# Optimization experiments

Hardware: AMD Instinct MI355X
Metric: run time of the kernel (lower is better)

Reference implementation:

```python
import jax, jax.numpy as jnp
import numpy as np

ALPHA_LO = float(np.exp(-1.0 / 5.0))   # 0.8187
ALPHA_HI = float(np.exp(-1.0 / 25.0))  # 0.9608
BN_EPS = 1e-5

B, T, D_IN, H = 32, 2000, 512, 512


def setup_inputs() -> dict:
    key = jax.random.key(0)
    ks = jax.random.split(key, 5)
    x = jax.random.normal(ks[0], (B, T, D_IN), dtype=jnp.float32)
    W = jax.random.normal(ks[1], (H, D_IN), dtype=jnp.float32) / np.sqrt(D_IN)
    b = jax.random.normal(ks[2], (H,), dtype=jnp.float32) * 0.01
    alpha = jax.random.uniform(ks[3], (H,), dtype=jnp.float32,
                               minval=ALPHA_LO, maxval=ALPHA_HI)
    gamma = jnp.ones((H,), dtype=jnp.float32)
    beta = jnp.zeros((H,), dtype=jnp.float32)
    ut0 = jax.random.uniform(ks[4], (B, H), dtype=jnp.float32)
    return {"x": x, "W": W, "b": b, "alpha": alpha,
            "gamma": gamma, "beta": beta, "ut0": ut0}


def reference(x, W, b, alpha, gamma, beta, ut0):
    # Linear: [B,T,Din] @ [Din,H] + b
    Wx = jnp.einsum("btd,hd->bth", x, W) + b
    # BatchNorm1d (training forward): stats over flattened (B*T) dim
    flat = Wx.reshape(-1, Wx.shape[-1])
    mean = flat.mean(axis=0)
    var = flat.var(axis=0)  # biased, as torch BN uses for normalization
    Wx = ((flat - mean) * jax.lax.rsqrt(var + BN_EPS) * gamma + beta).reshape(Wx.shape)
    # Readout cell: leaky integration + softmax accumulation over time
    a = jnp.clip(alpha, ALPHA_LO, ALPHA_HI)

    def step(carry, wxt):
        ut, acc = carry
        ut = a * ut + (1.0 - a) * wxt          # [B,H]
        acc = acc + jax.nn.softmax(ut, axis=1)
        return (ut, acc), None

    wx_t = jnp.transpose(Wx, (1, 0, 2))  # [T,B,H]
    (_, out), _ = jax.lax.scan(step, (ut0, jnp.zeros_like(ut0)), wx_t)
    return out[:, None, :]  # [B,1,H]
```

## Files before the change

### kernel.cpp

```cpp
#include <hip/hip_runtime.h>
#include <hip/hip_bf16.h>
#include <stdint.h>


namespace {
constexpr int kB = 32;
constexpr int kT = 2000;
constexpr int kD = 512;
constexpr int kH = 512;
constexpr int kM = kB * kT;
constexpr int kBM = 64;
constexpr int kNB = kM / kBM;
constexpr int kL = 16;
constexpr int kC = kT / kL;
constexpr int kG = 5;
constexpr int kNG = kC / kG;
constexpr float kALo = 0.81873075307798182f;
constexpr float kAHi = 0.96078943915232320f;

typedef __bf16 bf16x4 __attribute__((ext_vector_type(4)));
typedef __bf16 bf16x8 __attribute__((ext_vector_type(8)));
typedef float floatx16 __attribute__((ext_vector_type(16)));

__device__ __forceinline__ float bf2f(unsigned short u) {
  return __builtin_bit_cast(float, (unsigned)u << 16);
}
__device__ __forceinline__ float clipa(float a) {
  return fminf(fmaxf(a, kALo), kAHi);
}
__device__ __forceinline__ float pow16(float a) {
  const float a2 = a * a, a4 = a2 * a2, a8 = a4 * a4;
  return a8 * a8;
}

__global__ __launch_bounds__(256) void wcvt_k(const float* __restrict__ W,
                                              __bf16* __restrict__ Wbf) {
  const int t = blockIdx.x * 256 + threadIdx.x;
  const float4 a0 = ((const float4*)W)[t * 2];
  const float4 a1 = ((const float4*)W)[t * 2 + 1];
  bf16x8 v;
  v[0] = (__bf16)a0.x; v[1] = (__bf16)a0.y; v[2] = (__bf16)a0.z; v[3] = (__bf16)a0.w;
  v[4] = (__bf16)a1.x; v[5] = (__bf16)a1.y; v[6] = (__bf16)a1.z; v[7] = (__bf16)a1.w;
  const int h = t >> 6, k8 = t & 63;
  *(bf16x8*)(Wbf + ((size_t)k8 * 512 + h) * 8) = v;
}

__global__ __launch_bounds__(512, 4) void gemm_k(const float* __restrict__ X,
                                                 const __bf16* __restrict__ Wbf,
                                                 const float* __restrict__ alpha,
                                                 unsigned short* __restrict__ Wxb,
                                                 float* __restrict__ vbuf,
                                                 float* __restrict__ partial) {
  __shared__ alignas(16) __bf16 As2[2][4][65][8];
  __shared__ float sred[2][kH];
  const int tid = threadIdx.x;
  const size_t row0 = (size_t)blockIdx.x * kBM;
  const int w = tid >> 6, L = tid & 63;
  const int ct0 = w * 2;
  const int lhalf = L >> 5, l32 = L & 31;
  const int arow = tid >> 3, acol = (tid & 7) * 4;
  const int akq = acol >> 3, aoff = acol & 7;

  floatx16 acc[2][2] = {};
  const float* xptr = X + (row0 + arow) * kD + acol;
  const __bf16* bptr = Wbf + ((size_t)(ct0 * 32) + l32) * 8;

  float4 a0 = *(const float4*)xptr;
  {
    bf16x4 av;
    av[0] = (__bf16)a0.x; av[1] = (__bf16)a0.y;
    av[2] = (__bf16)a0.z; av[3] = (__bf16)a0.w;
    *(bf16x4*)&As2[0][akq][arow][aoff] = av;
  }
  a0 = *(const float4*)(xptr + 32);
  asm volatile("s_waitcnt lgkmcnt(0)" ::: "memory");
  __builtin_amdgcn_s_barrier();

#pragma unroll 1
  for (int s = 0; s < 16; ++s) {
    const int buf = s & 1;
    if (s < 15) {
      bf16x4 av;
      av[0] = (__bf16)a0.x; av[1] = (__bf16)a0.y;
      av[2] = (__bf16)a0.z; av[3] = (__bf16)a0.w;
      *(bf16x4*)&As2[buf ^ 1][akq][arow][aoff] = av;
      if (s < 14)
        a0 = *(const float4*)(xptr + (s + 2) * 32);
    }
#pragma unroll
    for (int kh = 0; kh < 2; ++kh) {
      const int kq = kh * 2 + lhalf;
      const __bf16* bq = bptr + (size_t)(s * 4 + kq) * 4096;
      const bf16x8 b0 = *(const bf16x8*)bq;
      const bf16x8 b1 = *(const bf16x8*)(bq + 256);
      const bf16x8 af0 = *(const bf16x8*)&As2[buf][kq][l32][0];
      const bf16x8 af1 = *(const bf16x8*)&As2[buf][kq][32 + l32][0];
      acc[0][0] = __builtin_amdgcn_mfma_f32_32x32x16_bf16(af0, b0, acc[0][0], 0, 0, 0);
      acc[0][1] = __builtin_amdgcn_mfma_f32_32x32x16_bf16(af0, b1, acc[0][1], 0, 0, 0);
      acc[1][0] = __builtin_amdgcn_mfma_f32_32x32x16_bf16(af1, b0, acc[1][0], 0, 0, 0);
      acc[1][1] = __builtin_amdgcn_mfma_f32_32x32x16_bf16(af1, b1, acc[1][1], 0, 0, 0);
    }
    if (s < 15) {
      asm volatile("s_waitcnt lgkmcnt(0)" ::: "memory");
      __builtin_amdgcn_s_barrier();
    }
  }

  __syncthreads();
  sred[0][tid] = 0.f;
  sred[1][tid] = 0.f;
  __syncthreads();
#pragma unroll
  for (int c = 0; c < 2; ++c) {
    float s = 0.f, q = 0.f;
#pragma unroll
    for (int rt = 0; rt < 2; ++rt) {
#pragma unroll
      for (int r = 0; r < 16; ++r) {
        const float v = acc[rt][c][r];
        s += v;
        q += v * v;
      }
    }
    s += __shfl_xor(s, 32);
    q += __shfl_xor(q, 32);
    if (lhalf == 0) {
      atomicAdd(&sred[0][(ct0 + c) * 32 + l32], s);
      atomicAdd(&sred[1][(ct0 + c) * 32 + l32], q);
    }
  }

#pragma unroll
  for (int c = 0; c < 2; ++c) {
    const int col = (ct0 + c) * 32 + l32;
    const float a = clipa(alpha[col]);
    const float oma = 1.0f - a;
    const float a2 = a * a, a4 = a2 * a2, a8 = a4 * a4;
    float wgt[8];
    wgt[0] = a8 * a2 * a; wgt[1] = a8 * a2; wgt[2] = a8 * a; wgt[3] = a8;
    wgt[4] = a2 * a;      wgt[5] = a2;      wgt[6] = a;      wgt[7] = 1.0f;
    const float mult = (lhalf == 0) ? a4 * oma : oma;
#pragma unroll
    for (int j = 0; j < 8; ++j) wgt[j] *= mult;
#pragma unroll
    for (int rt = 0; rt < 2; ++rt) {
#pragma unroll
      for (int c32 = 0; c32 < 2; ++c32) {
        float S = 0.f;
#pragma unroll
        for (int j = 0; j < 8; ++j) S += wgt[j] * acc[rt][c][c32 * 8 + j];
        S += __shfl_xor(S, 32);
        if (lhalf == 0) {
          const int g = (int)blockIdx.x * 4 + rt * 2 + c32;
          vbuf[(size_t)g * kH + col] = S;
        }
      }
    }
  }

#pragma unroll
  for (int rt = 0; rt < 2; ++rt) {
#pragma unroll
    for (int c = 0; c < 2; ++c) {
      const int col = (ct0 + c) * 32 + l32;
#pragma unroll
      for (int r = 0; r < 16; ++r) {
        const int row = rt * 32 + 4 * lhalf + (r & 3) + 8 * (r >> 2);
        const unsigned short u = __builtin_bit_cast(unsigned short, (__bf16)acc[rt][c][r]);
        const unsigned un = __shfl_down((unsigned)u, 1);
        if ((l32 & 1) == 0)
          *(unsigned*)(Wxb + (row0 + row) * (size_t)kH + col) = (unsigned)u | (un << 16);
      }
    }
  }
  __syncthreads();
  partial[(size_t)blockIdx.x * 1024 + tid] = sred[0][tid];
  partial[(size_t)blockIdx.x * 1024 + 512 + tid] = sred[1][tid];
}

__global__ __launch_bounds__(512) void red1_k(const float* __restrict__ partial,
                                              float* __restrict__ sums) {
  const int tid = threadIdx.x;
  const int r0 = blockIdx.x * 25;
  float s0 = 0.f, s1 = 0.f;
#pragma unroll 5
  for (int r = 0; r < 25; ++r) {
    s0 += partial[(size_t)(r0 + r) * 1024 + tid];
    s1 += partial[(size_t)(r0 + r) * 1024 + 512 + tid];
  }
  atomicAdd(&sums[tid], s0);
  atomicAdd(&sums[kH + tid], s1);
}

__global__ __launch_bounds__(512) void fin_scan_k(const float* __restrict__ sums,
                                                  const float* __restrict__ alpha,
                                                  const float* __restrict__ gamma,
                                                  const float* __restrict__ beta,
                                                  const float* __restrict__ ut0,
                                                  float* __restrict__ prm,
                                                  const float* __restrict__ vbuf,
                                                  float* __restrict__ ustart) {
  const int h = threadIdx.x;
  const int b = blockIdx.x;
  const float inv_n = 1.0f / (float)kM;
  const float mean = sums[h] * inv_n;
  const float var = sums[kH + h] * inv_n - mean * mean;
  const float sc = gamma[h] * rsqrtf(var + 1e-5f);
  const float sh = beta[h] - mean * sc;
  const float a = clipa(alpha[h]);
  if (b == 0) {
    prm[h] = sc;
    prm[kH + h] = sh;
    prm[2 * kH + h] = a;
    prm[3 * kH + h] = 1.0f - a;
  }
  const float a16 = pow16(a);
  const float shc = sh * (1.0f - a16);
  float u = ut0[(size_t)b * kH + h];
  float vc[kG];
#pragma unroll 1
  for (int cb = 0; cb < kC; cb += kG) {
#pragma unroll
    for (int j = 0; j < kG; ++j)
      vc[j] = vbuf[((size_t)b * kC + cb + j) * kH + h];
    ustart[((size_t)b * kNG + cb / kG) * kH + h] = u;
#pragma unroll
    for (int j = 0; j < kG; ++j) u = a16 * u + sc * vc[j] + shc;
  }
}

__global__ __launch_bounds__(512) void soft_k(const unsigned short* __restrict__ Wxb,
                                              const float* __restrict__ prm,
                                              const float* __restrict__ ustart,
                                              float* __restrict__ out) {
  __shared__ float part[kL][9];
  __shared__ float zinv[kL];
  const int bc = blockIdx.x;
  const int b = bc / kNG, grp = bc % kNG;
  const int h = threadIdx.x;
  const int wv = h >> 6, lane = h & 63;
  const float sc = prm[h], sh = prm[kH + h];
  const float a = prm[2 * kH + h], oma = prm[3 * kH + h];
  float u = ustart[(size_t)bc * kH + h];
  const unsigned short* base =
      Wxb + ((size_t)b * kT + (size_t)grp * kG * kL) * kH + h;
  float acc = 0.f;
#pragma unroll 1
  for (int cc = 0; cc < kG; ++cc) {
    float e[kL];
#pragma unroll
    for (int i = 0; i < kL; ++i) {
      const float wvx = bf2f(base[(size_t)(cc * kL + i) * kH]) * sc + sh;
      u = a * u + oma * wvx;
      e[i] = __expf(u);
    }
#pragma unroll
    for (int i = 0; i < kL; ++i) {
      float s = e[i];
#pragma unroll
      for (int off = 32; off > 0; off >>= 1) s += __shfl_xor(s, off);
      if (lane == 0) part[i][wv] = s;
    }
    __syncthreads();
    if (h < kL) {
      float s = 0.f;
#pragma unroll
      for (int j = 0; j < 8; ++j) s += part[h][j];
      zinv[h] = 1.0f / s;
    }
    __syncthreads();
#pragma unroll
    for (int i = 0; i < kL; ++i) acc += e[i] * zinv[i];
    __syncthreads();
  }
  atomicAdd(&out[(size_t)b * kH + h], acc);
}

}

extern "C" void kernel_launch(void* const* d_in, const int* in_sizes, int n_in,
                              void* d_out, int out_size, void* d_ws, size_t ws_size,
                              hipStream_t stream) {
  const float* x = (const float*)d_in[0];
  const float* Wm = (const float*)d_in[1];
  const float* alpha = (const float*)d_in[3];
  const float* gamma = (const float*)d_in[4];
  const float* beta = (const float*)d_in[5];
  const float* ut0 = (const float*)d_in[6];
  float* out = (float*)d_out;

  float* wsp = (float*)d_ws;
  float* vbuf = wsp;
  float* ustart = vbuf + (size_t)kB * kC * kH;
  float* partial = ustart + (size_t)kB * kNG * kH;
  float* sums = partial + (size_t)1000 * 1024;
  float* prm = sums + 2 * kH;
  __bf16* Wbf = (__bf16*)(prm + 4 * kH);
  unsigned short* Wxb = (unsigned short*)(Wbf + (size_t)kH * kD);

  hipMemsetAsync(sums, 0, 2 * kH * sizeof(float), stream);
  hipMemsetAsync(out, 0, (size_t)kB * kH * sizeof(float), stream);
  wcvt_k<<<128, 256, 0, stream>>>(Wm, Wbf);
  gemm_k<<<kNB, 512, 0, stream>>>(x, Wbf, alpha, Wxb, vbuf, partial);
  red1_k<<<40, 512, 0, stream>>>(partial, sums);
  fin_scan_k<<<kB, 512, 0, stream>>>(sums, alpha, gamma, beta, ut0, prm, vbuf, ustart);
  soft_k<<<kB * kNG, 512, 0, stream>>>(Wxb, prm, ustart, out);
}
```

Baseline: 304.8 us.

## Fuse reduction, scan and softmax into one cooperative kernel; fold memsets into conversion

Three tail kernels (stat reduction, per-batch chunk scan, softmax accumulation) are merged into one cooperative kernel with grid syncs, and each block now handles two chunk groups. The two memsets move into the weight-conversion kernel. The GEMM main loop is reorganised to unroll two K steps and prefetch two A tiles ahead. The intent is to cut launch overhead and inter-kernel gaps, at the cost of grid-sync latency, only 32 blocks active during the scan phase, and halved parallelism in the softmax phase.

```diff
diff --git a/kernel.cpp b/kernel.cpp
--- a/kernel.cpp
+++ b/kernel.cpp
@@ -1,6 +1,9 @@
 #include <hip/hip_runtime.h>
 #include <hip/hip_bf16.h>
+#include <hip/hip_cooperative_groups.h>
 #include <stdint.h>
+
+namespace cg = cooperative_groups;
 
 
 namespace {
@@ -34,8 +37,12 @@
 }
 
 __global__ __launch_bounds__(256) void wcvt_k(const float* __restrict__ W,
-                                              __bf16* __restrict__ Wbf) {
+                                              __bf16* __restrict__ Wbf,
+                                              float* __restrict__ sums,
+                                              float* __restrict__ out) {
   const int t = blockIdx.x * 256 + threadIdx.x;
+  if (t < 2 * kH) sums[t] = 0.f;
+  if (t < kB * kH) out[t] = 0.f;
   const float4 a0 = ((const float4*)W)[t * 2];
   const float4 a1 = ((const float4*)W)[t * 2 + 1];
   bf16x8 v;
@@ -65,42 +72,51 @@
   const float* xptr = X + (row0 + arow) * kD + acol;
   const __bf16* bptr = Wbf + ((size_t)(ct0 * 32) + l32) * 8;
 
-  float4 a0 = *(const float4*)xptr;
-  {
+  auto stage = [&](int bufIdx, const float4& a) {
     bf16x4 av;
-    av[0] = (__bf16)a0.x; av[1] = (__bf16)a0.y;
-    av[2] = (__bf16)a0.z; av[3] = (__bf16)a0.w;
-    *(bf16x4*)&As2[0][akq][arow][aoff] = av;
-  }
-  a0 = *(const float4*)(xptr + 32);
-  asm volatile("s_waitcnt lgkmcnt(0)" ::: "memory");
-  __builtin_amdgcn_s_barrier();
-
-#pragma unroll 1
-  for (int s = 0; s < 16; ++s) {
-    const int buf = s & 1;
-    if (s < 15) {
-      bf16x4 av;
-      av[0] = (__bf16)a0.x; av[1] = (__bf16)a0.y;
-      av[2] = (__bf16)a0.z; av[3] = (__bf16)a0.w;
-      *(bf16x4*)&As2[buf ^ 1][akq][arow][aoff] = av;
-      if (s < 14)
-        a0 = *(const float4*)(xptr + (s + 2) * 32);
-    }
+    av[0] = (__bf16)a.x; av[1] = (__bf16)a.y;
+    av[2] = (__bf16)a.z; av[3] = (__bf16)a.w;
+    *(bf16x4*)&As2[bufIdx][akq][arow][aoff] = av;
+  };
+  auto compute = [&](int s, int bufIdx) {
 #pragma unroll
     for (int kh = 0; kh < 2; ++kh) {
       const int kq = kh * 2 + lhalf;
       const __bf16* bq = bptr + (size_t)(s * 4 + kq) * 4096;
       const bf16x8 b0 = *(const bf16x8*)bq;
       const bf16x8 b1 = *(const bf16x8*)(bq + 256);
-      const bf16x8 af0 = *(const bf16x8*)&As2[buf][kq][l32][0];
-      const bf16x8 af1 = *(const bf16x8*)&As2[buf][kq][32 + l32][0];
+      const bf16x8 af0 = *(const bf16x8*)&As2[bufIdx][kq][l32][0];
+      const bf16x8 af1 = *(const bf16x8*)&As2[bufIdx][kq][32 + l32][0];
       acc[0][0] = __builtin_amdgcn_mfma_f32_32x32x16_bf16(af0, b0, acc[0][0], 0, 0, 0);
       acc[0][1] = __builtin_amdgcn_mfma_f32_32x32x16_bf16(af0, b1, acc[0][1], 0, 0, 0);
       acc[1][0] = __builtin_amdgcn_mfma_f32_32x32x16_bf16(af1, b0, acc[1][0], 0, 0, 0);
       acc[1][1] = __builtin_amdgcn_mfma_f32_32x32x16_bf16(af1, b1, acc[1][1], 0, 0, 0);
     }
-    if (s < 15) {
+  };
+
+  {
+    const float4 a0 = *(const float4*)xptr;
+    stage(0, a0);
+  }
+  float4 aA = *(const float4*)(xptr + 1 * 32);
+  float4 aB = *(const float4*)(xptr + 2 * 32);
+  asm volatile("s_waitcnt lgkmcnt(0)" ::: "memory");
+  __builtin_amdgcn_s_barrier();
+
+#pragma unroll 1
+  for (int s = 0; s < 16; s += 2) {
+    stage(1, aA);
+    if (s + 3 < 16) aA = *(const float4*)(xptr + (s + 3) * 32);
+    compute(s, 0);
+    asm volatile("s_waitcnt lgkmcnt(0)" ::: "memory");
+    __builtin_amdgcn_s_barrier();
+    const int o = s + 1;
+    if (o < 15) {
+      stage(0, aB);
+      if (o + 3 < 16) aB = *(const float4*)(xptr + (o + 3) * 32);
+    }
+    compute(o, 1);
+    if (o < 15) {
       asm volatile("s_waitcnt lgkmcnt(0)" ::: "memory");
       __builtin_amdgcn_s_barrier();
     }
@@ -178,102 +194,106 @@
   partial[(size_t)blockIdx.x * 1024 + 512 + tid] = sred[1][tid];
 }
 
-__global__ __launch_bounds__(512) void red1_k(const float* __restrict__ partial,
-                                              float* __restrict__ sums) {
+__global__ __launch_bounds__(512, 4) void tail_k(const float* __restrict__ partial,
+                                                 float* __restrict__ sums,
+                                                 const float* __restrict__ alpha,
+                                                 const float* __restrict__ gamma,
+                                                 const float* __restrict__ beta,
+                                                 const float* __restrict__ ut0,
+                                                 float* __restrict__ vbuf,
+                                                 float* __restrict__ ustart,
+                                                 const unsigned short* __restrict__ Wxb,
+                                                 float* __restrict__ out) {
+  cg::grid_group grid = cg::this_grid();
+  __shared__ float part[kL][9];
+  __shared__ float zinv[kL];
   const int tid = threadIdx.x;
-  const int r0 = blockIdx.x * 25;
-  float s0 = 0.f, s1 = 0.f;
+
+  if (blockIdx.x < 40) {
+    const int r0 = blockIdx.x * 25;
+    float s0 = 0.f, s1 = 0.f;
 #pragma unroll 5
-  for (int r = 0; r < 25; ++r) {
-    s0 += partial[(size_t)(r0 + r) * 1024 + tid];
-    s1 += partial[(size_t)(r0 + r) * 1024 + 512 + tid];
-  }
-  atomicAdd(&sums[tid], s0);
-  atomicAdd(&sums[kH + tid], s1);
-}
-
-__global__ __launch_bounds__(512) void fin_scan_k(const float* __restrict__ sums,
-                                                  const float* __restrict__ alpha,
-                                                  const float* __restrict__ gamma,
-                                                  const float* __restrict__ beta,
-                                                  const float* __restrict__ ut0,
-                                                  float* __restrict__ prm,
-                                                  const float* __restrict__ vbuf,
-                                                  float* __restrict__ ustart) {
-  const int h = threadIdx.x;
-  const int b = blockIdx.x;
+    for (int r = 0; r < 25; ++r) {
+      s0 += partial[(size_t)(r0 + r) * 1024 + tid];
+      s1 += partial[(size_t)(r0 + r) * 1024 + 512 + tid];
+    }
+    atomicAdd(&sums[tid], s0);
+    atomicAdd(&sums[kH + tid], s1);
+  }
+  __threadfence();
+  grid.sync();
+
+  if (blockIdx.x < kB) {
+    const int h = tid, b = blockIdx.x;
+    const float inv_n = 1.0f / (float)kM;
+    const float mean = sums[h] * inv_n;
+    const float var = sums[kH + h] * inv_n - mean * mean;
+    const float sc = gamma[h] * rsqrtf(var + 1e-5f);
+    const float sh = beta[h] - mean * sc;
+    const float a16 = pow16(clipa(alpha[h]));
+    const float shc = sh * (1.0f - a16);
+    float u = ut0[(size_t)b * kH + h];
+    float vc[kG];
+#pragma unroll 1
+    for (int cb = 0; cb < kC; cb += kG) {
+#pragma unroll
+      for (int j = 0; j < kG; ++j)
+        vc[j] = vbuf[((size_t)b * kC + cb + j) * kH + h];
+      ustart[((size_t)b * kNG + cb / kG) * kH + h] = u;
+#pragma unroll
+      for (int j = 0; j < kG; ++j) u = a16 * u + sc * vc[j] + shc;
+    }
+  }
+  __threadfence();
+  grid.sync();
+
+  const int h = tid;
+  const int wv = h >> 6, lane = h & 63;
   const float inv_n = 1.0f / (float)kM;
   const float mean = sums[h] * inv_n;
   const float var = sums[kH + h] * inv_n - mean * mean;
   const float sc = gamma[h] * rsqrtf(var + 1e-5f);
   const float sh = beta[h] - mean * sc;
   const float a = clipa(alpha[h]);
-  if (b == 0) {
-    prm[h] = sc;
-    prm[kH + h] = sh;
-    prm[2 * kH + h] = a;
-    prm[3 * kH + h] = 1.0f - a;
-  }
-  const float a16 = pow16(a);
-  const float shc = sh * (1.0f - a16);
-  float u = ut0[(size_t)b * kH + h];
-  float vc[kG];
+  const float oma = 1.0f - a;
 #pragma unroll 1
-  for (int cb = 0; cb < kC; cb += kG) {
-#pragma unroll
-    for (int j = 0; j < kG; ++j)
-      vc[j] = vbuf[((size_t)b * kC + cb + j) * kH + h];
-    ustart[((size_t)b * kNG + cb / kG) * kH + h] = u;
-#pragma unroll
-    for (int j = 0; j < kG; ++j) u = a16 * u + sc * vc[j] + shc;
-  }
-}
-
-__global__ __launch_bounds__(512) void soft_k(const unsigned short* __restrict__ Wxb,
-                                              const float* __restrict__ prm,
-                                              const float* __restrict__ ustart,
-                                              float* __restrict__ out) {
-  __shared__ float part[kL][9];
-  __shared__ float zinv[kL];
-  const int bc = blockIdx.x;
-  const int b = bc / kNG, grp = bc % kNG;
-  const int h = threadIdx.x;
-  const int wv = h >> 6, lane = h & 63;
-  const float sc = prm[h], sh = prm[kH + h];
-  const float a = prm[2 * kH + h], oma = prm[3 * kH + h];
-  float u = ustart[(size_t)bc * kH + h];
-  const unsigned short* base =
-      Wxb + ((size_t)b * kT + (size_t)grp * kG * kL) * kH + h;
-  float acc = 0.f;
+  for (int uu = 0; uu < 2; ++uu) {
+    const int bc = blockIdx.x * 2 + uu;
+    const int b = bc / kNG, grp = bc % kNG;
+    float u = ustart[(size_t)bc * kH + h];
+    const unsigned short* base =
+        Wxb + ((size_t)b * kT + (size_t)grp * kG * kL) * kH + h;
+    float acc = 0.f;
 #pragma unroll 1
-  for (int cc = 0; cc < kG; ++cc) {
-    float e[kL];
-#pragma unroll
-    for (int i = 0; i < kL; ++i) {
-      const float wvx = bf2f(base[(size_t)(cc * kL + i) * kH]) * sc + sh;
-      u = a * u + oma * wvx;
-      e[i] = __expf(u);
-    }
-#pragma unroll
-    for (int i = 0; i < kL; ++i) {
-      float s = e[i];
-#pragma unroll
-      for (int off = 32; off > 0; off >>= 1) s += __shfl_xor(s, off);
-      if (lane == 0) part[i][wv] = s;
-    }
-    __syncthreads();
-    if (h < kL) {
-      float s = 0.f;
-#pragma unroll
-      for (int j = 0; j < 8; ++j) s += part[h][j];
-      zinv[h] = 1.0f / s;
-    }
-    __syncthreads();
-#pragma unroll
-    for (int i = 0; i < kL; ++i) acc += e[i] * zinv[i];
-    __syncthreads();
-  }
-  atomicAdd(&out[(size_t)b * kH + h], acc);
+    for (int cc = 0; cc < kG; ++cc) {
+      float e[kL];
+#pragma unroll
+      for (int i = 0; i < kL; ++i) {
+        const float wvx = bf2f(base[(size_t)(cc * kL + i) * kH]) * sc + sh;
+        u = a * u + oma * wvx;
+        e[i] = __expf(u);
+      }
+#pragma unroll
+      for (int i = 0; i < kL; ++i) {
+        float s = e[i];
+#pragma unroll
+        for (int off = 32; off > 0; off >>= 1) s += __shfl_xor(s, off);
+        if (lane == 0) part[i][wv] = s;
+      }
+      __syncthreads();
+      if (h < kL) {
+        float s = 0.f;
+#pragma unroll
+        for (int j = 0; j < 8; ++j) s += part[h][j];
+        zinv[h] = 1.0f / s;
+      }
+      __syncthreads();
+#pragma unroll
+      for (int i = 0; i < kL; ++i) acc += e[i] * zinv[i];
+      __syncthreads();
+    }
+    atomicAdd(&out[(size_t)b * kH + h], acc);
+  }
 }
 
 }
@@ -294,15 +314,16 @@
   float* ustart = vbuf + (size_t)kB * kC * kH;
   float* partial = ustart + (size_t)kB * kNG * kH;
   float* sums = partial + (size_t)1000 * 1024;
-  float* prm = sums + 2 * kH;
-  __bf16* Wbf = (__bf16*)(prm + 4 * kH);
+  __bf16* Wbf = (__bf16*)(sums + 2 * kH);
   unsigned short* Wxb = (unsigned short*)(Wbf + (size_t)kH * kD);
 
-  hipMemsetAsync(sums, 0, 2 * kH * sizeof(float), stream);
-  hipMemsetAsync(out, 0, (size_t)kB * kH * sizeof(float), stream);
-  wcvt_k<<<128, 256, 0, stream>>>(Wm, Wbf);
+  wcvt_k<<<128, 256, 0, stream>>>(Wm, Wbf, sums, out);
   gemm_k<<<kNB, 512, 0, stream>>>(x, Wbf, alpha, Wxb, vbuf, partial);
-  red1_k<<<40, 512, 0, stream>>>(partial, sums);
-  fin_scan_k<<<kB, 512, 0, stream>>>(sums, alpha, gamma, beta, ut0, prm, vbuf, ustart);
-  soft_k<<<kB * kNG, 512, 0, stream>>>(Wxb, prm, ustart, out);
-}
+
+  const unsigned short* WxbC = Wxb;
+  void* targs[] = {(void*)&partial, (void*)&sums,  (void*)&alpha, (void*)&gamma,
+                   (void*)&beta,    (void*)&ut0,   (void*)&vbuf,  (void*)&ustart,
+                   (void*)&WxbC,    (void*)&out};
+  hipLaunchCooperativeKernel((const void*)tail_k, dim3(400), dim3(512), targs, 0,
+                             stream);
+}
```

Result: slower. 491.3 us (+61.2%).

## Prefetch B fragments into registers and fold memsets into weight-convert kernel

Applied to the files above, without the earlier changes.

The GEMM main loop is unrolled by two, with ping-pong register buffers for the W fragments, so the B loads for the next k-step are issued before the current MFMAs. The X prefetch is also deepened to two float4 stages ahead. The two hipMemsetAsync calls are removed and their zeroing is done inside wcvt_k, which saves two launches. The cost is higher register pressure: eight extra bf16x8 registers per thread under launch_bounds(512,4).

```diff
diff --git a/kernel.cpp b/kernel.cpp
--- a/kernel.cpp
+++ b/kernel.cpp
@@ -34,8 +34,12 @@
 }
 
 __global__ __launch_bounds__(256) void wcvt_k(const float* __restrict__ W,
-                                              __bf16* __restrict__ Wbf) {
+                                              __bf16* __restrict__ Wbf,
+                                              float* __restrict__ sums,
+                                              float* __restrict__ out) {
   const int t = blockIdx.x * 256 + threadIdx.x;
+  if (t < 2 * kH) sums[t] = 0.f;
+  if (t < kB * kH) out[t] = 0.f;
   const float4 a0 = ((const float4*)W)[t * 2];
   const float4 a1 = ((const float4*)W)[t * 2 + 1];
   bf16x8 v;
@@ -65,42 +69,61 @@
   const float* xptr = X + (row0 + arow) * kD + acol;
   const __bf16* bptr = Wbf + ((size_t)(ct0 * 32) + l32) * 8;
 
-  float4 a0 = *(const float4*)xptr;
-  {
-    bf16x4 av;
-    av[0] = (__bf16)a0.x; av[1] = (__bf16)a0.y;
-    av[2] = (__bf16)a0.z; av[3] = (__bf16)a0.w;
-    *(bf16x4*)&As2[0][akq][arow][aoff] = av;
-  }
-  a0 = *(const float4*)(xptr + 32);
-  asm volatile("s_waitcnt lgkmcnt(0)" ::: "memory");
-  __builtin_amdgcn_s_barrier();
-
-#pragma unroll 1
-  for (int s = 0; s < 16; ++s) {
-    const int buf = s & 1;
-    if (s < 15) {
-      bf16x4 av;
-      av[0] = (__bf16)a0.x; av[1] = (__bf16)a0.y;
-      av[2] = (__bf16)a0.z; av[3] = (__bf16)a0.w;
-      *(bf16x4*)&As2[buf ^ 1][akq][arow][aoff] = av;
-      if (s < 14)
-        a0 = *(const float4*)(xptr + (s + 2) * 32);
-    }
+  bf16x8 bE[4], bO[4];
+  auto loadB = [&](bf16x8* dst, int s) {
 #pragma unroll
     for (int kh = 0; kh < 2; ++kh) {
       const int kq = kh * 2 + lhalf;
       const __bf16* bq = bptr + (size_t)(s * 4 + kq) * 4096;
-      const bf16x8 b0 = *(const bf16x8*)bq;
-      const bf16x8 b1 = *(const bf16x8*)(bq + 256);
-      const bf16x8 af0 = *(const bf16x8*)&As2[buf][kq][l32][0];
-      const bf16x8 af1 = *(const bf16x8*)&As2[buf][kq][32 + l32][0];
-      acc[0][0] = __builtin_amdgcn_mfma_f32_32x32x16_bf16(af0, b0, acc[0][0], 0, 0, 0);
-      acc[0][1] = __builtin_amdgcn_mfma_f32_32x32x16_bf16(af0, b1, acc[0][1], 0, 0, 0);
-      acc[1][0] = __builtin_amdgcn_mfma_f32_32x32x16_bf16(af1, b0, acc[1][0], 0, 0, 0);
-      acc[1][1] = __builtin_amdgcn_mfma_f32_32x32x16_bf16(af1, b1, acc[1][1], 0, 0, 0);
-    }
-    if (s < 15) {
+      dst[kh * 2 + 0] = *(const bf16x8*)bq;
+      dst[kh * 2 + 1] = *(const bf16x8*)(bq + 256);
+    }
+  };
+  auto stage = [&](int bufIdx, const float4& a) {
+    bf16x4 av;
+    av[0] = (__bf16)a.x; av[1] = (__bf16)a.y;
+    av[2] = (__bf16)a.z; av[3] = (__bf16)a.w;
+    *(bf16x4*)&As2[bufIdx][akq][arow][aoff] = av;
+  };
+  auto computeR = [&](int bufIdx, const bf16x8* bb) {
+#pragma unroll
+    for (int kh = 0; kh < 2; ++kh) {
+      const int kq = kh * 2 + lhalf;
+      const bf16x8 af0 = *(const bf16x8*)&As2[bufIdx][kq][l32][0];
+      const bf16x8 af1 = *(const bf16x8*)&As2[bufIdx][kq][32 + l32][0];
+      acc[0][0] = __builtin_amdgcn_mfma_f32_32x32x16_bf16(af0, bb[kh * 2 + 0], acc[0][0], 0, 0, 0);
+      acc[0][1] = __builtin_amdgcn_mfma_f32_32x32x16_bf16(af0, bb[kh * 2 + 1], acc[0][1], 0, 0, 0);
+      acc[1][0] = __builtin_amdgcn_mfma_f32_32x32x16_bf16(af1, bb[kh * 2 + 0], acc[1][0], 0, 0, 0);
+      acc[1][1] = __builtin_amdgcn_mfma_f32_32x32x16_bf16(af1, bb[kh * 2 + 1], acc[1][1], 0, 0, 0);
+    }
+  };
+
+  loadB(bE, 0);
+  {
+    const float4 a0 = *(const float4*)xptr;
+    stage(0, a0);
+  }
+  float4 aA = *(const float4*)(xptr + 1 * 32);
+  float4 aB = *(const float4*)(xptr + 2 * 32);
+  asm volatile("s_waitcnt lgkmcnt(0)" ::: "memory");
+  __builtin_amdgcn_s_barrier();
+
+#pragma unroll 1
+  for (int s = 0; s < 16; s += 2) {
+    loadB(bO, s + 1);
+    stage(1, aA);
+    if (s + 3 < 16) aA = *(const float4*)(xptr + (s + 3) * 32);
+    computeR(0, bE);
+    asm volatile("s_waitcnt lgkmcnt(0)" ::: "memory");
+    __builtin_amdgcn_s_barrier();
+    const int o = s + 1;
+    if (o < 15) {
+      loadB(bE, o + 1);
+      stage(0, aB);
+      if (o + 3 < 16) aB = *(const float4*)(xptr + (o + 3) * 32);
+    }
+    computeR(1, bO);
+    if (o < 15) {
       asm volatile("s_waitcnt lgkmcnt(0)" ::: "memory");
       __builtin_amdgcn_s_barrier();
     }
@@ -298,9 +321,7 @@
   __bf16* Wbf = (__bf16*)(prm + 4 * kH);
   unsigned short* Wxb = (unsigned short*)(Wbf + (size_t)kH * kD);
 
-  hipMemsetAsync(sums, 0, 2 * kH * sizeof(float), stream);
-  hipMemsetAsync(out, 0, (size_t)kB * kH * sizeof(float), stream);
-  wcvt_k<<<128, 256, 0, stream>>>(Wm, Wbf);
+  wcvt_k<<<128, 256, 0, stream>>>(Wm, Wbf, sums, out);
   gemm_k<<<kNB, 512, 0, stream>>>(x, Wbf, alpha, Wxb, vbuf, partial);
   red1_k<<<40, 512, 0, stream>>>(partial, sums);
   fin_scan_k<<<kB, 512, 0, stream>>>(sums, alpha, gamma, beta, ut0, prm, vbuf, ustart);
```

Result: no change. 302.9 us (-0.6%).
